# Kernel optimization log

Measured on AMD Instinct MI355X. Metric: run time of the kernel, lower is better.

The kernel has to match this reference:

```python
import jax, jax.numpy as jnp
import numpy as np

B, K, V = 64, 8, 128000

def setup_inputs() -> dict:
    key = jax.random.key(0)
    ks = jax.random.split(key, 6)
    # probs are normalized distributions over the vocab, as produced by softmax upstream
    draft_probs = jax.nn.softmax(jax.random.normal(ks[0], (B, K, V), dtype=jnp.float32), axis=-1)
    oracle_probs = jax.nn.softmax(jax.random.normal(ks[1], (B, K + 1, V), dtype=jnp.float32), axis=-1)
    draft_tokens = jax.random.randint(ks[2], (B, K), 0, V, dtype=jnp.int32)
    oracle_tokens = jax.random.randint(ks[3], (B, K), 0, V, dtype=jnp.int32)
    uniforms = jax.random.uniform(ks[4], (B, K), dtype=jnp.float32)   # accept/reject draws (torch.rand per step)
    sample_u = jax.random.uniform(ks[5], (B,), dtype=jnp.float32)     # draw for residual/bonus sample
    return {
        'draft_tokens': draft_tokens,
        'draft_probs': draft_probs,
        'oracle_tokens': oracle_tokens,
        'oracle_probs': oracle_probs,
        'uniforms': uniforms,
        'sample_u': sample_u,
        'num_draft_tokens': K,
    }

def reference(draft_tokens, draft_probs, oracle_tokens, oracle_probs, uniforms, sample_u, num_draft_tokens):
    # Parallel-prefix formulation of the sequential accept/reject loop.
    Kd = num_draft_tokens
    bidx = jnp.arange(draft_probs.shape[0])
    # p_draft[i] = draft_probs[i, draft_token_i], p_oracle[i] = oracle_probs[i, draft_token_i]
    p_d = jnp.take_along_axis(draft_probs, draft_tokens[..., None], axis=-1)[..., 0]          # [B,K]
    p_o = jnp.take_along_axis(oracle_probs[:, :Kd], draft_tokens[..., None], axis=-1)[..., 0]  # [B,K]
    accept_prob = jnp.minimum(1.0, p_o / p_d)                                                  # [B,K]
    accept = uniforms < accept_prob                                                            # [B,K]
    # number of accepted tokens = length of leading run of accepts (loop breaks at first reject)
    prefix = jnp.cumprod(accept.astype(jnp.int32), axis=1)
    num_accepted = prefix.sum(axis=1)                                                          # [B]
    all_accepted = num_accepted == Kd
    # residual distribution at the first rejected position r (clipped when all accepted)
    r = jnp.minimum(num_accepted, Kd - 1)
    o_r = oracle_probs[bidx, r]                                                                # [B,V]
    d_r = draft_probs[bidx, r]                                                                 # [B,V]
    residual = jnp.maximum(o_r - d_r, 0.0)
    residual = residual / residual.sum(axis=-1, keepdims=True)
    bonus_dist = oracle_probs[:, Kd]                                                           # [B,V]
    final_dist = jnp.where(all_accepted[:, None], bonus_dist, residual)
    # inverse-CDF sample of the replacement/bonus token
    cdf = jnp.cumsum(final_dist, axis=-1)
    new_token = jnp.minimum(jnp.sum(cdf < sample_u[:, None], axis=-1), final_dist.shape[-1] - 1).astype(jnp.int32)
    # pack accepted prefix + sampled token, pad with -1 to fixed length K+1
    pos = jnp.arange(Kd + 1)[None, :]
    draft_pad = jnp.pad(draft_tokens, ((0, 0), (0, 1)))
    tokens = jnp.where(pos < num_accepted[:, None], draft_pad,
                       jnp.where(pos == num_accepted[:, None], new_token[:, None], -1)).astype(jnp.int32)
    return tokens, num_accepted
```

## Files before the change

### kernel.cpp

```cpp
#include <hip/hip_runtime.h>

#define B 64
#define K 8
#define V 128000
#define CH 4096
#define NCH 32

__global__ __launch_bounds__(64) void k1_accept(
    const int*   __restrict__ draft_tokens,
    const float* __restrict__ draft_probs,
    const float* __restrict__ oracle_probs,
    const float* __restrict__ uniforms,
    int* __restrict__ meta,
    int* __restrict__ out_na)
{
  int b = threadIdx.x;
  if (b >= B) return;
  int na = 0;
  for (int k = 0; k < K; ++k) {
    int t   = draft_tokens[b * K + k];
    float pd = draft_probs [((size_t)(b * K       + k)) * V + t];
    float po = oracle_probs[((size_t)(b * (K + 1) + k)) * V + t];
    float ap = fminf(1.0f, po / pd);
    if (uniforms[b * K + k] < ap) na++; else break;
  }
  meta[b]   = na;
  out_na[b] = na;
}

__global__ __launch_bounds__(256) void k2_sums(
    const float* __restrict__ draft_probs,
    const float* __restrict__ oracle_probs,
    const int*   __restrict__ meta,
    float* __restrict__ chunkSums)
{
  const int b = blockIdx.x >> 5;
  const int c = blockIdx.x & 31;
  const int na  = meta[b];
  const bool acc = (na == K);
  const int row = acc ? K : na;
  const float* orow = oracle_probs + ((size_t)(b * (K + 1) + row)) * V;
  const float* drow = draft_probs  + ((size_t)(b * K       + row)) * V;

  const int base = c * CH;
  float s = 0.f;
#pragma unroll
  for (int it = 0; it < 4; ++it) {
    int idx = base + it * 1024 + (int)threadIdx.x * 4;
    if (idx < V) {
      float4 o = *(const float4*)(orow + idx);
      if (acc) {
        s += (o.x + o.y) + (o.z + o.w);
      } else {
        float4 d = *(const float4*)(drow + idx);
        s += fmaxf(o.x - d.x, 0.f) + fmaxf(o.y - d.y, 0.f)
           + fmaxf(o.z - d.z, 0.f) + fmaxf(o.w - d.w, 0.f);
      }
    }
  }
  for (int off = 32; off > 0; off >>= 1) s += __shfl_down(s, off);
  __shared__ float wsum[4];
  int lane = threadIdx.x & 63, w = threadIdx.x >> 6;
  if (lane == 0) wsum[w] = s;
  __syncthreads();
  if (threadIdx.x == 0)
    chunkSums[b * NCH + c] = (wsum[0] + wsum[1]) + (wsum[2] + wsum[3]);
}

__global__ __launch_bounds__(256) void k3_sample(
    const int*   __restrict__ draft_tokens,
    const float* __restrict__ draft_probs,
    const float* __restrict__ oracle_probs,
    const float* __restrict__ sample_u,
    const int*   __restrict__ meta,
    const float* __restrict__ chunkSums,
    int* __restrict__ out_tokens)
{
  const int b    = blockIdx.x;
  const int tid  = threadIdx.x;
  const int lane = tid & 63, w = tid >> 6;

  const int na   = meta[b];
  const bool acc = (na == K);
  const int row  = acc ? K : na;
  const float* orow = oracle_probs + ((size_t)(b * (K + 1) + row)) * V;
  const float* drow = draft_probs  + ((size_t)(b * K       + row)) * V;

  __shared__ float sT, sBase;
  __shared__ int   sC, sIdx;
  __shared__ float sWS[4];

  if (w == 0) {
    float v = (lane < NCH) ? chunkSums[b * NCH + lane] : 0.f;
    float incl = v;
    for (int off = 1; off < NCH; off <<= 1) {
      float n = __shfl_up(incl, off);
      if (lane >= off) incl += n;
    }
    float S = __shfl(incl, NCH - 1);
    float T = acc ? sample_u[b] : sample_u[b] * S;
    unsigned long long m = __ballot(lane < NCH && incl >= T);
    if (lane == 0) {
      sT = T;
      if (m == 0ULL) { sC = -1; sIdx = V - 1; sBase = 0.f; }
    }
    if (m != 0ULL) {
      int cstar = __ffsll((long long)m) - 1;
      if (lane == cstar) {
        sC = cstar;
        sBase = incl - v;
        int fb = cstar * CH + CH - 1;
        sIdx = fb < V ? fb : V - 1;
      }
    }
  }
  __syncthreads();

  const int cstar = sC;
  int new_token;
  if (cstar >= 0) {
    const float T = sT;
    const int base = cstar * CH;
    const int estart = base + tid * 16;
    float vals[16];
    float s = 0.f;
#pragma unroll
    for (int j4 = 0; j4 < 4; ++j4) {
      int idx = estart + j4 * 4;
      float4 o = make_float4(0.f, 0.f, 0.f, 0.f);
      float4 d = make_float4(0.f, 0.f, 0.f, 0.f);
      if (idx < V) {
        o = *(const float4*)(orow + idx);
        if (!acc) d = *(const float4*)(drow + idx);
      }
      float v0 = acc ? o.x : fmaxf(o.x - d.x, 0.f);
      float v1 = acc ? o.y : fmaxf(o.y - d.y, 0.f);
      float v2 = acc ? o.z : fmaxf(o.z - d.z, 0.f);
      float v3 = acc ? o.w : fmaxf(o.w - d.w, 0.f);
      vals[j4 * 4 + 0] = v0; vals[j4 * 4 + 1] = v1;
      vals[j4 * 4 + 2] = v2; vals[j4 * 4 + 3] = v3;
      s += (v0 + v1) + (v2 + v3);
    }
    float incl = s;
    for (int off = 1; off < 64; off <<= 1) {
      float n = __shfl_up(incl, off);
      if (lane >= off) incl += n;
    }
    if (lane == 63) sWS[w] = incl;
    __syncthreads();
    float woff = 0.f;
    for (int i = 0; i < w; ++i) woff += sWS[i];
    float run = sBase + woff + (incl - s);
    int found = -1;
#pragma unroll
    for (int j = 0; j < 16; ++j) {
      run += vals[j];
      if (found < 0 && run >= T) found = estart + j;
    }
    if (found >= 0 && found < V) atomicMin(&sIdx, found);
    __syncthreads();
    new_token = sIdx;
  } else {
    new_token = V - 1;
  }

  if (tid < K + 1) {
    int pos = tid, val;
    if (pos < na)       val = draft_tokens[b * K + pos];
    else if (pos == na) val = new_token;
    else                val = -1;
    out_tokens[b * (K + 1) + pos] = val;
  }
}

extern "C" void kernel_launch(void* const* d_in, const int* in_sizes, int n_in,
                              void* d_out, int out_size, void* d_ws, size_t ws_size,
                              hipStream_t stream) {
  const int*   draft_tokens = (const int*)  d_in[0];
  const float* draft_probs  = (const float*)d_in[1];
  const float* oracle_probs = (const float*)d_in[3];
  const float* uniforms     = (const float*)d_in[4];
  const float* sample_u     = (const float*)d_in[5];

  int* out_tokens = (int*)d_out;
  int* out_na     = out_tokens + B * (K + 1);

  float* chunkSums = (float*)d_ws;
  int*   meta      = (int*)d_ws + B * NCH;

  k1_accept<<<1, 64, 0, stream>>>(draft_tokens, draft_probs, oracle_probs,
                                  uniforms, meta, out_na);
  k2_sums<<<B * NCH, 256, 0, stream>>>(draft_probs, oracle_probs, meta, chunkSums);
  k3_sample<<<B, 256, 0, stream>>>(draft_tokens, draft_probs, oracle_probs,
                                   sample_u, meta, chunkSums, out_tokens);
}
```

Baseline: 455.2 us.

## Fuse accept, chunk-sum and sampling kernels via last-block atomic counter

Merges the three kernels into one. Each block recomputes the per-batch accepted count with a wave ballot, computes its chunk sum, and increments a per-batch counter. The last block for each batch then performs the prefix scan and inverse-CDF sampling. This removes the intermediate launches and the dependency stalls between them, at the cost of a memset launch, redundant accept computation in every block, and an atomic handoff between blocks.

```diff
diff --git a/kernel.cpp b/kernel.cpp
--- a/kernel.cpp
+++ b/kernel.cpp
@@ -6,39 +6,45 @@
 #define CH 4096
 #define NCH 32
 
-__global__ __launch_bounds__(64) void k1_accept(
+__global__ __launch_bounds__(256) void rs_fused(
     const int*   __restrict__ draft_tokens,
     const float* __restrict__ draft_probs,
     const float* __restrict__ oracle_probs,
     const float* __restrict__ uniforms,
-    int* __restrict__ meta,
-    int* __restrict__ out_na)
+    const float* __restrict__ sample_u,
+    int*   __restrict__ done,
+    float* __restrict__ chunkSums,
+    int*   __restrict__ out_tokens,
+    int*   __restrict__ out_na)
 {
-  int b = threadIdx.x;
-  if (b >= B) return;
-  int na = 0;
-  for (int k = 0; k < K; ++k) {
-    int t   = draft_tokens[b * K + k];
-    float pd = draft_probs [((size_t)(b * K       + k)) * V + t];
-    float po = oracle_probs[((size_t)(b * (K + 1) + k)) * V + t];
-    float ap = fminf(1.0f, po / pd);
-    if (uniforms[b * K + k] < ap) na++; else break;
+  const int b    = blockIdx.x >> 5;
+  const int c    = blockIdx.x & 31;
+  const int tid  = threadIdx.x;
+  const int lane = tid & 63, w = tid >> 6;
+
+  __shared__ int   s_na;
+  __shared__ int   s_last;
+  __shared__ float sWS[4];
+  __shared__ float sT, sBase;
+  __shared__ int   sC, sIdx;
+
+  if (w == 0) {
+    int accept = 0;
+    if (lane < K) {
+      int   t  = draft_tokens[b * K + lane];
+      float pd = draft_probs [((size_t)(b * K       + lane)) * V + t];
+      float po = oracle_probs[((size_t)(b * (K + 1) + lane)) * V + t];
+      accept = (uniforms[b * K + lane] < fminf(1.0f, po / pd)) ? 1 : 0;
+    }
+    unsigned long long m    = __ballot(accept != 0) & 0xFFull;
+    unsigned long long notm = (~m) & 0xFFull;
+    int na = notm ? (int)__builtin_ctzll(notm) : K;
+    if (lane == 0) s_na = na;
   }
-  meta[b]   = na;
-  out_na[b] = na;
-}
-
-__global__ __launch_bounds__(256) void k2_sums(
-    const float* __restrict__ draft_probs,
-    const float* __restrict__ oracle_probs,
-    const int*   __restrict__ meta,
-    float* __restrict__ chunkSums)
-{
-  const int b = blockIdx.x >> 5;
-  const int c = blockIdx.x & 31;
-  const int na  = meta[b];
+  __syncthreads();
+  const int  na  = s_na;
   const bool acc = (na == K);
-  const int row = acc ? K : na;
+  const int  row = acc ? K : na;
   const float* orow = oracle_probs + ((size_t)(b * (K + 1) + row)) * V;
   const float* drow = draft_probs  + ((size_t)(b * K       + row)) * V;
 
@@ -46,7 +52,7 @@
   float s = 0.f;
 #pragma unroll
   for (int it = 0; it < 4; ++it) {
-    int idx = base + it * 1024 + (int)threadIdx.x * 4;
+    int idx = base + it * 1024 + tid * 4;
     if (idx < V) {
       float4 o = *(const float4*)(orow + idx);
       if (acc) {
@@ -59,39 +65,25 @@
     }
   }
   for (int off = 32; off > 0; off >>= 1) s += __shfl_down(s, off);
-  __shared__ float wsum[4];
-  int lane = threadIdx.x & 63, w = threadIdx.x >> 6;
-  if (lane == 0) wsum[w] = s;
+  if (lane == 0) sWS[w] = s;
   __syncthreads();
-  if (threadIdx.x == 0)
-    chunkSums[b * NCH + c] = (wsum[0] + wsum[1]) + (wsum[2] + wsum[3]);
-}
-
-__global__ __launch_bounds__(256) void k3_sample(
-    const int*   __restrict__ draft_tokens,
-    const float* __restrict__ draft_probs,
-    const float* __restrict__ oracle_probs,
-    const float* __restrict__ sample_u,
-    const int*   __restrict__ meta,
-    const float* __restrict__ chunkSums,
-    int* __restrict__ out_tokens)
-{
-  const int b    = blockIdx.x;
-  const int tid  = threadIdx.x;
-  const int lane = tid & 63, w = tid >> 6;
-
-  const int na   = meta[b];
-  const bool acc = (na == K);
-  const int row  = acc ? K : na;
-  const float* orow = oracle_probs + ((size_t)(b * (K + 1) + row)) * V;
-  const float* drow = draft_probs  + ((size_t)(b * K       + row)) * V;
-
-  __shared__ float sT, sBase;
-  __shared__ int   sC, sIdx;
-  __shared__ float sWS[4];
+  if (tid == 0) {
+    float total = (sWS[0] + sWS[1]) + (sWS[2] + sWS[3]);
+    __hip_atomic_store(&chunkSums[b * NCH + c], total,
+                       __ATOMIC_RELAXED, __HIP_MEMORY_SCOPE_AGENT);
+    int old = __hip_atomic_fetch_add(&done[b], 1,
+                                     __ATOMIC_ACQ_REL, __HIP_MEMORY_SCOPE_AGENT);
+    s_last = (old == NCH - 1);
+    if (c == 0) out_na[b] = na;
+  }
+  __syncthreads();
+  if (!s_last) return;
 
   if (w == 0) {
-    float v = (lane < NCH) ? chunkSums[b * NCH + lane] : 0.f;
+    float v = (lane < NCH)
+      ? __hip_atomic_load(&chunkSums[b * NCH + lane],
+                          __ATOMIC_RELAXED, __HIP_MEMORY_SCOPE_AGENT)
+      : 0.f;
     float incl = v;
     for (int off = 1; off < NCH; off <<= 1) {
       float n = __shfl_up(incl, off);
@@ -105,11 +97,11 @@
       if (m == 0ULL) { sC = -1; sIdx = V - 1; sBase = 0.f; }
     }
     if (m != 0ULL) {
-      int cstar = __ffsll((long long)m) - 1;
-      if (lane == cstar) {
-        sC = cstar;
+      int cs = (int)__builtin_ctzll(m);
+      if (lane == cs) {
+        sC = cs;
         sBase = incl - v;
-        int fb = cstar * CH + CH - 1;
+        int fb = cs * CH + CH - 1;
         sIdx = fb < V ? fb : V - 1;
       }
     }
@@ -120,10 +112,10 @@
   int new_token;
   if (cstar >= 0) {
     const float T = sT;
-    const int base = cstar * CH;
-    const int estart = base + tid * 16;
+    const int cbase  = cstar * CH;
+    const int estart = cbase + tid * 16;
     float vals[16];
-    float s = 0.f;
+    float ps = 0.f;
 #pragma unroll
     for (int j4 = 0; j4 < 4; ++j4) {
       int idx = estart + j4 * 4;
@@ -139,9 +131,9 @@
       float v3 = acc ? o.w : fmaxf(o.w - d.w, 0.f);
       vals[j4 * 4 + 0] = v0; vals[j4 * 4 + 1] = v1;
       vals[j4 * 4 + 2] = v2; vals[j4 * 4 + 3] = v3;
-      s += (v0 + v1) + (v2 + v3);
+      ps += (v0 + v1) + (v2 + v3);
     }
-    float incl = s;
+    float incl = ps;
     for (int off = 1; off < 64; off <<= 1) {
       float n = __shfl_up(incl, off);
       if (lane >= off) incl += n;
@@ -150,7 +142,7 @@
     __syncthreads();
     float woff = 0.f;
     for (int i = 0; i < w; ++i) woff += sWS[i];
-    float run = sBase + woff + (incl - s);
+    float run = sBase + woff + (incl - ps);
     int found = -1;
 #pragma unroll
     for (int j = 0; j < 16; ++j) {
@@ -185,12 +177,11 @@
   int* out_tokens = (int*)d_out;
   int* out_na     = out_tokens + B * (K + 1);
 
-  float* chunkSums = (float*)d_ws;
-  int*   meta      = (int*)d_ws + B * NCH;
+  int*   done      = (int*)d_ws;
+  float* chunkSums = (float*)d_ws + B;
 
-  k1_accept<<<1, 64, 0, stream>>>(draft_tokens, draft_probs, oracle_probs,
-                                  uniforms, meta, out_na);
-  k2_sums<<<B * NCH, 256, 0, stream>>>(draft_probs, oracle_probs, meta, chunkSums);
-  k3_sample<<<B, 256, 0, stream>>>(draft_tokens, draft_probs, oracle_probs,
-                                   sample_u, meta, chunkSums, out_tokens);
+  hipMemsetAsync(done, 0, B * sizeof(int), stream);
+  rs_fused<<<B * NCH, 256, 0, stream>>>(draft_tokens, draft_probs, oracle_probs,
+                                        uniforms, sample_u, done, chunkSums,
+                                        out_tokens, out_na);
 }
```

After: 528.6 us. +16.1%, slower.
